# Performance work log

Measured on AMD Instinct MI355X. Metric: run time of the kernel, lower is better.

## Reference

```python
import jax, jax.numpy as jnp
import numpy as np

B, L, D = 1, 2048, 1024
H, E = 16, 64        # n_heads, d_head
ROT = E // 2         # rotary half-dim
FF = 4 * D
EPS = 1e-6
NEG = -1e30


def setup_inputs() -> dict:
    key = jax.random.key(0)
    ks = jax.random.split(key, 6)
    x = jax.random.normal(ks[0], (B, L, D), jnp.float32)
    theta = jax.random.uniform(ks[1], (B, H, L, ROT), jnp.float32) * (2.0 * np.pi)
    scale = jax.random.normal(ks[2], (B, D), jnp.float32) * 0.1
    w_in = jax.random.normal(ks[3], (7 * D, D), jnp.float32) * (D ** -0.5)
    w_out = jax.random.normal(ks[4], (D, 5 * D), jnp.float32) * ((5 * D) ** -0.5)
    attn_scale = jnp.full((2, H), 10.0, jnp.float32)
    return {"x": x, "theta": theta, "scale": scale,
            "w_in": w_in, "w_out": w_out, "attn_scale": attn_scale}


def _rope(t, cos, sin):
    # t: [b,h,l,E]; rotary applied to first 2*ROT dims (== E here, so no passthrough)
    t1, t2 = t[..., :ROT], t[..., ROT:2 * ROT]
    return jnp.concatenate([t1 * cos - t2 * sin, t2 * cos + t1 * sin], axis=-1)


def _forward(x, theta, scale, w_in, w_out, attn_scale):
    b, l, d = x.shape
    skip = x
    # AdaRMSNorm (no learned weight): rms-normalize then modulate by (1 + scale)
    xn = x * jax.lax.rsqrt(jnp.mean(x ** 2, axis=-1, keepdims=True) + EPS)
    xn = xn * (1.0 + scale[:, None, :])
    # fused QKV + MLP-up projection (torch Linear: y = x @ W.T)
    proj = jnp.einsum('bld,fd->blf', xn, w_in)       # [b,l,7d]
    qkv, up = proj[..., :3 * d], proj[..., 3 * d:]
    up = jax.nn.gelu(up, approximate=True)           # GELU(tanh)
    # 'b l (t nh e) -> t b nh l e'
    qkv = qkv.reshape(b, l, 3, H, E).transpose(2, 0, 3, 1, 4)
    q, k, v = qkv[0], qkv[1], qkv[2]
    # cosine-sim rescaling: q_h * sqrt(s_h)/||q||, k_h * sqrt(s_h)/||k||
    s = jnp.sqrt(attn_scale[0])[None, :, None, None]
    q = q * (s * jax.lax.rsqrt(jnp.sum(q ** 2, axis=-1, keepdims=True) + EPS))
    k = k * (s * jax.lax.rsqrt(jnp.sum(k ** 2, axis=-1, keepdims=True) + EPS))
    # rotary embedding
    cos, sin = jnp.cos(theta), jnp.sin(theta)
    q, k = _rope(q, cos, sin), _rope(k, cos, sin)
    # causal attention with scale = 1.0 (cosine-sim path)
    scores = jnp.einsum('bhqe,bhke->bhqk', q, k)
    causal = jnp.tril(jnp.ones((l, l), bool))
    scores = jnp.where(causal[None, None], scores, NEG)
    probs = jax.nn.softmax(scores, axis=-1)
    attn = jnp.einsum('bhqk,bhke->bhqe', probs, v)
    attn_out = attn.transpose(0, 2, 1, 3).reshape(b, l, d)  # 'b nh l e -> b l (nh e)'
    h = jnp.concatenate([attn_out, up], axis=-1)            # [b,l,5d]
    return jnp.einsum('blf,df->bld', h, w_out) + skip


def reference(x, theta, scale, w_in, w_out, attn_scale):
    return _forward(x, theta, scale, w_in, w_out, attn_scale)
```

## Files before the change

kernel.cpp:

```cpp
#include <hip/hip_runtime.h>

typedef unsigned short u16;
typedef unsigned int u32;
typedef __attribute__((ext_vector_type(8))) short bf16x8;
typedef __attribute__((ext_vector_type(8))) unsigned short u16x8;
typedef __attribute__((ext_vector_type(4))) float f32x4;
typedef __attribute__((ext_vector_type(16))) float f32x16;

#define L_SEQ 2048
#define DMODEL 1024
#define NHEAD 16
#define EHEAD 64
#define FPROJ 7168
#define FCAT 5120
#define NEGINF -1e30f
#define LOG2E 1.44269504088896f
#define EXP2F(x) __builtin_amdgcn_exp2f(x)

__device__ __forceinline__ u16 f2bf(float f) {
  union { float f; u32 u; } v; v.f = f;
  u32 r = v.u + 0x7FFFu + ((v.u >> 16) & 1u);
  return (u16)(r >> 16);
}
__device__ __forceinline__ float bf2f(u16 h) {
  union { u32 u; float f; } v; v.u = ((u32)h) << 16;
  return v.f;
}
__device__ __forceinline__ float gelu_f(float x) {
  float y = 0.7978845608028654f * (x + 0.044715f * x * x * x);
  float t = __expf(-2.0f * fabsf(y));
  float th = (1.0f - t) / (1.0f + t);
  th = (y < 0.0f) ? -th : th;
  return 0.5f * x * (1.0f + th);
}
__device__ __forceinline__ void gld16(void* lds, const void* g) {
  __builtin_amdgcn_global_load_lds((const __attribute__((address_space(1))) u32*)g,
                                   (__attribute__((address_space(3))) u32*)lds, 16, 0, 0);
}

__global__ __launch_bounds__(256) void cvt2_kernel(const float* __restrict__ a,
                                                   u16* __restrict__ oa, int na4,
                                                   const float* __restrict__ b,
                                                   u16* __restrict__ ob, int nb4) {
  int i = blockIdx.x * 256 + threadIdx.x;
  const float* src;
  u16* dst;
  int j;
  if (i < na4) {
    src = a; dst = oa; j = i;
  } else {
    j = i - na4;
    if (j >= nb4) return;
    src = b; dst = ob;
  }
  float4 v = ((const float4*)src)[j];
  ((u32*)dst)[2 * j] = (u32)f2bf(v.x) | ((u32)f2bf(v.y) << 16);
  ((u32*)dst)[2 * j + 1] = (u32)f2bf(v.z) | ((u32)f2bf(v.w) << 16);
}

__global__ __launch_bounds__(256) void rmsnorm_kernel(const float* __restrict__ x,
                                                      const float* __restrict__ scale,
                                                      u16* __restrict__ xn) {
  int row = blockIdx.x;
  const float4 v = ((const float4*)(x + (size_t)row * DMODEL))[threadIdx.x];
  float ss = v.x * v.x + v.y * v.y + v.z * v.z + v.w * v.w;
#pragma unroll
  for (int m = 1; m < 64; m <<= 1) ss += __shfl_xor(ss, m);
  __shared__ float ws[4];
  if ((threadIdx.x & 63) == 0) ws[threadIdx.x >> 6] = ss;
  __syncthreads();
  float tot = ws[0] + ws[1] + ws[2] + ws[3];
  float r = rsqrtf(tot * (1.0f / DMODEL) + 1e-6f);
  float4 sc = ((const float4*)scale)[threadIdx.x];
  u32 w0 = (u32)f2bf(v.x * r * (1.0f + sc.x)) | ((u32)f2bf(v.y * r * (1.0f + sc.y)) << 16);
  u32 w1 = (u32)f2bf(v.z * r * (1.0f + sc.z)) | ((u32)f2bf(v.w * r * (1.0f + sc.w)) << 16);
  u32* dst = (u32*)(xn + (size_t)row * DMODEL);
  dst[2 * threadIdx.x] = w0;
  dst[2 * threadIdx.x + 1] = w1;
}

__device__ __forceinline__ void stage_half(u16* lds, const u16* g, int K, int tid) {
#pragma unroll
  for (int i = 0; i < 2; ++i) {
    int idx = tid + i * 512;
    int r = idx >> 3;
    int gcb = ((idx & 7) << 4) ^ ((r & 7) << 4);
    gld16((char*)lds + idx * 16, (const char*)g + (size_t)r * K * 2 + gcb);
  }
}

#define GFENCE asm volatile("" ::: "memory")
#define VMW0 asm volatile("s_waitcnt vmcnt(0)" ::: "memory")
#define VMW2 asm volatile("s_waitcnt vmcnt(2)" ::: "memory")
#define ST_A(BUF, T, HALF) stage_half(sA + (BUF) * 16384 + (HALF) * 8192, \
    Ab + (size_t)((HALF) * 128) * K + (T) * 64, K, tid)
#define ST_B(BUF, T, HALF) stage_half(sB + (BUF) * 16384 + (HALF) * 8192, \
    Bb + (size_t)((HALF) * 128) * K + (T) * 64, K, tid)

#define PHASE(HM, KH, BUFB, DOVM, STCODE) do { \
    const char* ab_ = (const char*)sA + (BUFB) * 32768 + (HM) * 16384 + frow * 128 + ((KH) ? co1 : co0); \
    const char* bb_ = (const char*)sB + (BUFB) * 32768 + (wn * 32 + frow) * 128 + ((KH) ? co1 : co0); \
    bf16x8 af_[8], bv_[2]; \
    _Pragma("unroll") \
    for (int mr = 0; mr < 8; ++mr) af_[mr] = *(const bf16x8*)(ab_ + mr * 2048); \
    bv_[0] = *(const bf16x8*)(bb_); \
    bv_[1] = *(const bf16x8*)(bb_ + 2048); \
    GFENCE; \
    STCODE; \
    if (DOVM) VMW2; \
    __builtin_amdgcn_s_barrier(); \
    __builtin_amdgcn_s_setprio(1); \
    _Pragma("unroll") \
    for (int mr = 0; mr < 8; ++mr) { \
      acc[(HM) * 8 + mr][0] = __builtin_amdgcn_mfma_f32_16x16x32_bf16(af_[mr], bv_[0], acc[(HM) * 8 + mr][0], 0, 0, 0); \
      acc[(HM) * 8 + mr][1] = __builtin_amdgcn_mfma_f32_16x16x32_bf16(af_[mr], bv_[1], acc[(HM) * 8 + mr][1], 0, 0, 0); \
    } \
    __builtin_amdgcn_s_setprio(0); \
    __builtin_amdgcn_s_barrier(); \
  } while (0)

template <int OUTMODE>
__global__ __launch_bounds__(512, 2) void gemm256(const u16* __restrict__ A,
                                                  const u16* __restrict__ B,
                                                  u16* __restrict__ C0,
                                                  u16* __restrict__ C1,
                                                  int M, int N, int K) {
  __shared__ __align__(16) u16 smem[65536];
  u16* const sA = smem;
  u16* const sB = smem + 32768;
  const int tid = threadIdx.x;
  const int lane = tid & 63;
  const int wn = tid >> 6;
  const int frow = lane & 15;
  const int kbyte = ((lane >> 4) & 3) << 4;
  const int sw = (frow & 7) << 4;
  const int co0 = kbyte ^ sw;
  const int co1 = (64 | kbyte) ^ sw;

  const int nbx = N >> 8;
  const int nbm = (int)gridDim.x / nbx;
  const int v = (blockIdx.x & 7) * ((int)gridDim.x >> 3) + ((int)blockIdx.x >> 3);
  const int bm = v % nbm, bn = v / nbm;
  const int kper = K / (int)gridDim.y;
  const int kbeg = blockIdx.y * kper;
  const u16* Ab = A + (size_t)(bm * 256) * K + kbeg;
  const u16* Bb = B + (size_t)(bn * 256) * K + kbeg;

  f32x4 acc[16][2] = {};

  const int NT = kper >> 6;
  ST_A(0, 0, 0); ST_B(0, 0, 0); ST_B(0, 0, 1); ST_A(0, 0, 1); ST_A(1, 1, 0);
  VMW2;
  __builtin_amdgcn_s_barrier();

  for (int kt = 0; kt < NT; kt += 2) {
    const int t1 = kt + 1;
    const int t2 = (kt + 2 >= NT) ? kt + 2 - NT : kt + 2;
    const int t3 = (kt + 3 >= NT) ? kt + 3 - NT : kt + 3;
    PHASE(0, 0, 0, 0, ST_B(1, t1, 0));
    PHASE(0, 1, 0, 0, ST_B(1, t1, 1));
    PHASE(1, 0, 0, 0, ST_A(1, t1, 1));
    PHASE(1, 1, 0, 1, ST_A(0, t2, 0));
    PHASE(0, 0, 1, 0, ST_B(0, t2, 0));
    PHASE(0, 1, 1, 0, ST_B(0, t2, 1));
    PHASE(1, 0, 1, 0, ST_A(0, t2, 1));
    PHASE(1, 1, 1, 1, ST_A(1, t3, 0));
  }

  VMW0;
  __syncthreads();

  const int lr0 = (lane >> 4) * 4;
  const bool up = (OUTMODE == 1) && (bn >= 12);
  u16* const Cp2 = (OUTMODE == 2) ? C0 + (size_t)blockIdx.y * M * N : nullptr;

#pragma unroll
  for (int hm = 0; hm < 2; ++hm) {
#pragma unroll
    for (int m8 = 0; m8 < 8; ++m8) {
#pragma unroll
      for (int nr = 0; nr < 2; ++nr) {
        int col = wn * 32 + nr * 16 + frow;
#pragma unroll
        for (int r = 0; r < 4; ++r) {
          float vv = acc[hm * 8 + m8][nr][r];
          smem[(m8 * 16 + lr0 + r) * 272 + col] = f2bf(up ? gelu_f(vv) : vv);
        }
      }
    }
    __syncthreads();
#pragma unroll
    for (int j = 0; j < 8; ++j) {
      int row = j * 16 + (tid >> 5);
      int c16 = (tid & 31) * 8;
      u16x8 vv = *(const u16x8*)&smem[row * 272 + c16];
      int gr = bm * 256 + hm * 128 + row;
      int gc = bn * 256 + c16;
      if (OUTMODE == 1) {
        if (!up) *(u16x8*)(C0 + (size_t)gr * (3 * DMODEL) + gc) = vv;
        else     *(u16x8*)(C1 + (size_t)gr * FCAT + (gc - 2048)) = vv;
      } else {
        *(u16x8*)(Cp2 + (size_t)gr * N + gc) = vv;
      }
    }
    __syncthreads();
  }
}

__global__ __launch_bounds__(256) void combine8(const u16* __restrict__ part,
                                                const float* __restrict__ x,
                                                float* __restrict__ out) {
  size_t i = (size_t)(blockIdx.x * 256 + threadIdx.x) * 8;
  float4 x0 = *(const float4*)(x + i);
  float4 x1 = *(const float4*)(x + i + 4);
  float s[8] = {x0.x, x0.y, x0.z, x0.w, x1.x, x1.y, x1.z, x1.w};
#pragma unroll
  for (int p = 0; p < 8; ++p) {
    u16x8 v = *(const u16x8*)(part + (size_t)p * (L_SEQ * DMODEL) + i);
#pragma unroll
    for (int j = 0; j < 8; ++j) s[j] += bf2f(v[j]);
  }
  float4 o0 = {s[0], s[1], s[2], s[3]};
  float4 o1 = {s[4], s[5], s[6], s[7]};
  *(float4*)(out + i) = o0;
  *(float4*)(out + i + 4) = o1;
}

__global__ __launch_bounds__(256) void qkv_prep(const u16* __restrict__ proj,
                                                const float* __restrict__ theta,
                                                const float* __restrict__ attn_scale,
                                                u16* __restrict__ qb, u16* __restrict__ kb,
                                                u16* __restrict__ vb) {
  const int l = blockIdx.x * 4 + (threadIdx.x >> 6);
  const int hd = blockIdx.y;
  const int e = threadIdx.x & 63;
  const u16* pr = proj + (size_t)l * (3 * DMODEL) + hd * EHEAD + e;
  float q = bf2f(pr[0]);
  float k = bf2f(pr[DMODEL]);
  float v = bf2f(pr[2 * DMODEL]);
  float sq = q * q, sk = k * k;
#pragma unroll
  for (int m = 1; m < 64; m <<= 1) {
    sq += __shfl_xor(sq, m);
    sk += __shfl_xor(sk, m);
  }
  float s = sqrtf(attn_scale[hd]);
  q *= LOG2E * s * rsqrtf(sq + 1e-6f);
  k *= s * rsqrtf(sk + 1e-6f);
  float ang = theta[((size_t)hd * L_SEQ + l) * 32 + (e & 31)];
  float cs = __cosf(ang), sn = __sinf(ang);
  float qp = __shfl_xor(q, 32), kp = __shfl_xor(k, 32);
  float qr = (e < 32) ? (q * cs - qp * sn) : (q * cs + qp * sn);
  float kr = (e < 32) ? (k * cs - kp * sn) : (k * cs + kp * sn);
  size_t o = ((size_t)hd * L_SEQ + l) * EHEAD + e;
  qb[o] = f2bf(qr);
  kb[o] = f2bf(kr);
  vb[o] = f2bf(v);
}

__global__ __launch_bounds__(128, 4) void attn_kernel(const u16* __restrict__ qb,
                                                      const u16* __restrict__ kb,
                                                      const u16* __restrict__ vb,
                                                      u16* __restrict__ po,
                                                      float* __restrict__ pm,
                                                      float* __restrict__ pl) {
  const int bid = blockIdx.x;
  const int s = 31 - (bid >> 6);
  const int hd = (bid >> 2) & 15;
  const int c = bid & 3;
  const int tid = threadIdx.x;
  const int lane = tid & 63;
  const int w = tid >> 6;
  const int h = lane >> 5;
  const int ql = lane & 31;
  const int qg = s * 64 + w * 32 + ql;
  const int nt = s + 1;
  const int t0 = (c * nt) >> 2;
  const int t1 = ((c + 1) * nt) >> 2;

  __shared__ u16 sK[64 * 64];
  __shared__ u16 sVT[64 * 64];

  const u16* Kh = kb + (size_t)hd * L_SEQ * EHEAD;
  const u16* Vh = vb + (size_t)hd * L_SEQ * EHEAD;
  const u16* Qh = qb + (size_t)hd * L_SEQ * EHEAD;

  bf16x8 qf[4];
#pragma unroll
  for (int es = 0; es < 4; ++es)
    qf[es] = *(const bf16x8*)(Qh + (size_t)qg * EHEAD + es * 16 + h * 8);

  f32x16 oa[2] = {};
  float m = NEGINF, lsum = 0.0f;

  const int vk = (tid & 15) * 4;
  const int ve = (tid >> 4) * 8;

  for (int kt = t0; kt < t1; ++kt) {
    const int k0 = kt * 64;
    __syncthreads();
#pragma unroll
    for (int i = 0; i < 4; ++i) {
      int r = w * 32 + i * 8 + (lane >> 3);
      const u16* src = Kh + (size_t)(k0 + r) * EHEAD + (((lane & 7) ^ (r & 7)) << 3);
      gld16(sK + (w * 32 + i * 8) * 64 + lane * 8, src);
    }
    u16x8 vr[4];
#pragma unroll
    for (int j = 0; j < 4; ++j)
      vr[j] = *(const u16x8*)(Vh + (size_t)(k0 + vk + j) * EHEAD + ve);
#pragma unroll
    for (int e = 0; e < 8; ++e) {
      int row = ve + e;
      int boff = row * 128 + ((((vk >> 3) ^ (row & 7)) << 4) | ((vk & 4) << 1));
      ushort4 pv;
      pv.x = vr[0][e]; pv.y = vr[1][e]; pv.z = vr[2][e]; pv.w = vr[3][e];
      *(ushort4*)((char*)sVT + boff) = pv;
    }
    __syncthreads();

    f32x16 st[2];
#pragma unroll
    for (int t = 0; t < 2; ++t) {
      f32x16 a = {};
      __builtin_amdgcn_s_setprio(1);
#pragma unroll
      for (int es = 0; es < 4; ++es) {
        int row = t * 32 + ql;
        int boff = row * 128 + (((es * 2 + h) ^ (row & 7)) << 4);
        bf16x8 kf = *(const bf16x8*)((const char*)sK + boff);
        a = __builtin_amdgcn_mfma_f32_32x32x16_bf16(kf, qf[es], a, 0, 0, 0);
      }
      __builtin_amdgcn_s_setprio(0);
      st[t] = a;
    }

    float p[2][16];
    float mx = NEGINF;
    const bool edge = (kt == s);
#pragma unroll
    for (int t = 0; t < 2; ++t)
#pragma unroll
      for (int r = 0; r < 16; ++r) {
        float v = st[t][r];
        if (edge) {
          int kg = k0 + t * 32 + (r & 3) + ((r >> 2) << 3) + h * 4;
          v = (kg > qg) ? NEGINF : v;
        }
        p[t][r] = v;
        mx = fmaxf(mx, v);
      }
    mx = fmaxf(mx, __shfl_xor(mx, 32));
    if (!__all(mx - m <= 8.0f)) {
      float mnew = fmaxf(m, mx);
      float alpha = EXP2F(m - mnew);
      lsum *= alpha;
#pragma unroll
      for (int et = 0; et < 2; ++et)
#pragma unroll
        for (int r = 0; r < 16; ++r) oa[et][r] *= alpha;
      m = mnew;
    }
    float ps = 0.0f;
#pragma unroll
    for (int t = 0; t < 2; ++t)
#pragma unroll
      for (int r = 0; r < 16; ++r) {
        float e_ = EXP2F(p[t][r] - m);
        p[t][r] = e_;
        ps += e_;
      }
    ps += __shfl_xor(ps, 32);
    lsum += ps;

    u32 pk_[2][8];
#pragma unroll
    for (int t = 0; t < 2; ++t)
#pragma unroll
      for (int i = 0; i < 8; ++i)
        asm("v_cvt_pk_bf16_f32 %0, %1, %2" : "=v"(pk_[t][i]) : "v"(p[t][2 * i]), "v"(p[t][2 * i + 1]));

#pragma unroll
    for (int ks = 0; ks < 4; ++ks) {
      const int tp = ks >> 1, base = (ks & 1) * 4;
      u32 s0 = h ? pk_[tp][base + 0] : pk_[tp][base + 2];
      u32 s1 = h ? pk_[tp][base + 1] : pk_[tp][base + 3];
      u32 r0 = (u32)__shfl_xor((int)s0, 32);
      u32 r1 = (u32)__shfl_xor((int)s1, 32);
      union { u32 u[4]; bf16x8 v; } pf;
      pf.u[0] = h ? r0 : pk_[tp][base + 0];
      pf.u[1] = h ? r1 : pk_[tp][base + 1];
      pf.u[2] = h ? pk_[tp][base + 2] : r0;
      pf.u[3] = h ? pk_[tp][base + 3] : r1;
      __builtin_amdgcn_s_setprio(1);
#pragma unroll
      for (int et = 0; et < 2; ++et) {
        int row = et * 32 + ql;
        int boff = row * 128 + (((ks * 2 + h) ^ (row & 7)) << 4);
        bf16x8 vf = *(const bf16x8*)((const char*)sVT + boff);
        oa[et] = __builtin_amdgcn_mfma_f32_32x32x16_bf16(vf, pf.v, oa[et], 0, 0, 0);
      }
      __builtin_amdgcn_s_setprio(0);
    }
  }

  const size_t pidx = (size_t)(s * 16 + hd) * 4 + c;
  u16* orow = po + pidx * 4096 + (size_t)(w * 32 + ql) * 64;
#pragma unroll
  for (int et = 0; et < 2; ++et)
#pragma unroll
    for (int g = 0; g < 4; ++g) {
      ushort4 ov;
      ov.x = f2bf(oa[et][4 * g + 0]);
      ov.y = f2bf(oa[et][4 * g + 1]);
      ov.z = f2bf(oa[et][4 * g + 2]);
      ov.w = f2bf(oa[et][4 * g + 3]);
      *(ushort4*)(orow + et * 32 + g * 8 + h * 4) = ov;
    }
  if (h == 0) {
    pm[pidx * 64 + w * 32 + ql] = m;
    pl[pidx * 64 + w * 32 + ql] = lsum;
  }
}

__global__ __launch_bounds__(256) void attn_merge(const u16* __restrict__ po,
                                                  const float* __restrict__ pm,
                                                  const float* __restrict__ pl,
                                                  u16* __restrict__ hb) {
  const int sh = blockIdx.x;
  const int s = sh >> 4, hd = sh & 15;
  const int r = threadIdx.x >> 2;
  const int ec = (threadIdx.x & 3) << 4;
  float mc[4], wgt[4];
  float M = NEGINF;
#pragma unroll
  for (int c = 0; c < 4; ++c) {
    mc[c] = pm[(size_t)(sh * 4 + c) * 64 + r];
    M = fmaxf(M, mc[c]);
  }
  float L = 0.0f;
#pragma unroll
  for (int c = 0; c < 4; ++c) {
    wgt[c] = EXP2F(mc[c] - M);
    L += pl[(size_t)(sh * 4 + c) * 64 + r] * wgt[c];
  }
  float inv = 1.0f / L;
  float o[16] = {};
#pragma unroll
  for (int c = 0; c < 4; ++c) {
    const u16* pp = po + (size_t)(sh * 4 + c) * 4096 + r * 64 + ec;
    u16x8 v0 = *(const u16x8*)pp;
    u16x8 v1 = *(const u16x8*)(pp + 8);
#pragma unroll
    for (int j = 0; j < 8; ++j) {
      o[j] += wgt[c] * bf2f(v0[j]);
      o[8 + j] += wgt[c] * bf2f(v1[j]);
    }
  }
  u16* dst = hb + (size_t)(s * 64 + r) * FCAT + hd * EHEAD + ec;
  u16x8 out0, out1;
#pragma unroll
  for (int j = 0; j < 8; ++j) {
    out0[j] = f2bf(o[j] * inv);
    out1[j] = f2bf(o[8 + j] * inv);
  }
  *(u16x8*)dst = out0;
  *(u16x8*)(dst + 8) = out1;
}

extern "C" void kernel_launch(void* const* d_in, const int* in_sizes, int n_in,
                              void* d_out, int out_size, void* d_ws, size_t ws_size,
                              hipStream_t stream) {
  const float* x = (const float*)d_in[0];
  const float* theta = (const float*)d_in[1];
  const float* scale = (const float*)d_in[2];
  const float* w_in = (const float*)d_in[3];
  const float* w_out = (const float*)d_in[4];
  const float* attn_scale = (const float*)d_in[5];
  float* out = (float*)d_out;

  char* ws = (char*)d_ws;
  u16* w_out_b = (u16*)ws;   ws += (size_t)DMODEL * FCAT * 2;
  u16* hb = (u16*)ws;        ws += (size_t)L_SEQ * FCAT * 2;
  u16* xn = (u16*)ws;        ws += (size_t)L_SEQ * DMODEL * 2;
  u16* w_in_b = (u16*)ws;    ws += (size_t)FPROJ * DMODEL * 2;
  u16* proj = (u16*)ws;      ws += (size_t)L_SEQ * 3 * DMODEL * 2;
  u16* qb = (u16*)ws;        ws += (size_t)NHEAD * L_SEQ * EHEAD * 2;
  u16* kb = (u16*)ws;        ws += (size_t)NHEAD * L_SEQ * EHEAD * 2;
  u16* vb = (u16*)ws;        ws += (size_t)NHEAD * L_SEQ * EHEAD * 2;
  u16* po = xn;
  float* pm = (float*)(po + (size_t)512 * 4 * 4096);
  float* pl = pm + 512 * 4 * 64;
  u16* part = xn;

  const int na4 = FPROJ * DMODEL / 4, nb4 = DMODEL * FCAT / 4;
  cvt2_kernel<<<(na4 + nb4 + 255) / 256, 256, 0, stream>>>(w_in, w_in_b, na4,
                                                           w_out, w_out_b, nb4);
  rmsnorm_kernel<<<L_SEQ, 256, 0, stream>>>(x, scale, xn);
  gemm256<1><<<(L_SEQ / 256) * (FPROJ / 256), 512, 0, stream>>>(xn, w_in_b, proj, hb,
                                                                L_SEQ, FPROJ, DMODEL);
  qkv_prep<<<dim3(L_SEQ / 4, NHEAD), 256, 0, stream>>>(proj, theta, attn_scale, qb, kb, vb);
  attn_kernel<<<2048, 128, 0, stream>>>(qb, kb, vb, po, pm, pl);
  attn_merge<<<512, 256, 0, stream>>>(po, pm, pl, hb);
  gemm256<2><<<dim3((L_SEQ / 256) * (DMODEL / 256), 8), 512, 0, stream>>>(hb, w_out_b, part,
                                                                          nullptr, L_SEQ, DMODEL, FCAT);
  combine8<<<L_SEQ * DMODEL / 8 / 256, 256, 0, stream>>>(part, x, out);
}
```

Before: 138.9 us.

## Fuse QKV norm, RoPE and head split into projection GEMM epilogue

Removes the separate qkv_prep kernel and the intermediate proj buffer. The QKV GEMM epilogue now computes per-head L2 normalisation, scaling and rotary directly from the LDS-staged tile and writes q/k/v in head-major layout. A sin/cos table is built from theta inside the weight-conversion kernel, so the epilogue only reads precomputed pairs. This saves a launch and a round trip of the projection through global memory. In exchange the epilogue gets heavier, each thread processes a whole 64-wide row with a 64-element local array, which may raise register pressure, and the float2 table adds a 16 MB write and later read.

```diff
diff --git a/kernel.cpp b/kernel.cpp
--- a/kernel.cpp
+++ b/kernel.cpp
@@ -38,24 +38,36 @@
                                    (__attribute__((address_space(3))) u32*)lds, 16, 0, 0);
 }
 
-__global__ __launch_bounds__(256) void cvt2_kernel(const float* __restrict__ a,
+__global__ __launch_bounds__(256) void cvt3_kernel(const float* __restrict__ a,
                                                    u16* __restrict__ oa, int na4,
                                                    const float* __restrict__ b,
-                                                   u16* __restrict__ ob, int nb4) {
+                                                   u16* __restrict__ ob, int nb4,
+                                                   const float* __restrict__ theta,
+                                                   float2* __restrict__ tab, int nt4) {
   int i = blockIdx.x * 256 + threadIdx.x;
-  const float* src;
-  u16* dst;
-  int j;
-  if (i < na4) {
-    src = a; dst = oa; j = i;
-  } else {
-    j = i - na4;
-    if (j >= nb4) return;
-    src = b; dst = ob;
-  }
-  float4 v = ((const float4*)src)[j];
-  ((u32*)dst)[2 * j] = (u32)f2bf(v.x) | ((u32)f2bf(v.y) << 16);
-  ((u32*)dst)[2 * j + 1] = (u32)f2bf(v.z) | ((u32)f2bf(v.w) << 16);
+  if (i < na4 + nb4) {
+    const float* src;
+    u16* dst;
+    int j;
+    if (i < na4) { src = a; dst = oa; j = i; }
+    else         { src = b; dst = ob; j = i - na4; }
+    float4 v = ((const float4*)src)[j];
+    ((u32*)dst)[2 * j] = (u32)f2bf(v.x) | ((u32)f2bf(v.y) << 16);
+    ((u32*)dst)[2 * j + 1] = (u32)f2bf(v.z) | ((u32)f2bf(v.w) << 16);
+    return;
+  }
+  int j = i - na4 - nb4;
+  if (j >= nt4) return;
+  float4 t = ((const float4*)theta)[j];
+  float2 o0, o1, o2, o3;
+  __sincosf(t.x, &o0.y, &o0.x);
+  __sincosf(t.y, &o1.y, &o1.x);
+  __sincosf(t.z, &o2.y, &o2.x);
+  __sincosf(t.w, &o3.y, &o3.x);
+  tab[4 * j + 0] = o0;
+  tab[4 * j + 1] = o1;
+  tab[4 * j + 2] = o2;
+  tab[4 * j + 3] = o3;
 }
 
 __global__ __launch_bounds__(256) void rmsnorm_kernel(const float* __restrict__ x,
@@ -124,6 +136,11 @@
                                                   const u16* __restrict__ B,
                                                   u16* __restrict__ C0,
                                                   u16* __restrict__ C1,
+                                                  u16* __restrict__ qb,
+                                                  u16* __restrict__ kb,
+                                                  u16* __restrict__ vb,
+                                                  const float2* __restrict__ tab,
+                                                  const float* __restrict__ ascale,
                                                   int M, int N, int K) {
   __shared__ __align__(16) u16 smem[65536];
   u16* const sA = smem;
@@ -170,7 +187,6 @@
   VMW0;
   __syncthreads();
 
-  const int lr0 = (lane >> 4) * 4;
   const bool up = (OUTMODE == 1) && (bn >= 12);
   u16* const Cp2 = (OUTMODE == 2) ? C0 + (size_t)blockIdx.y * M * N : nullptr;
 
@@ -184,24 +200,68 @@
 #pragma unroll
         for (int r = 0; r < 4; ++r) {
           float vv = acc[hm * 8 + m8][nr][r];
-          smem[(m8 * 16 + lr0 + r) * 272 + col] = f2bf(up ? gelu_f(vv) : vv);
+          smem[(m8 * 16 + ((lane >> 4) * 4) + r) * 272 + col] = f2bf(up ? gelu_f(vv) : vv);
         }
       }
     }
     __syncthreads();
-#pragma unroll
-    for (int j = 0; j < 8; ++j) {
-      int row = j * 16 + (tid >> 5);
-      int c16 = (tid & 31) * 8;
-      u16x8 vv = *(const u16x8*)&smem[row * 272 + c16];
-      int gr = bm * 256 + hm * 128 + row;
-      int gc = bn * 256 + c16;
-      if (OUTMODE == 1) {
-        if (!up) *(u16x8*)(C0 + (size_t)gr * (3 * DMODEL) + gc) = vv;
-        else     *(u16x8*)(C1 + (size_t)gr * FCAT + (gc - 2048)) = vv;
-      } else {
-        *(u16x8*)(Cp2 + (size_t)gr * N + gc) = vv;
-      }
+
+    if (OUTMODE == 2) {
+#pragma unroll
+      for (int j = 0; j < 8; ++j) {
+        int row = j * 16 + (tid >> 5);
+        int c16 = (tid & 31) * 8;
+        u16x8 vv = *(const u16x8*)&smem[row * 272 + c16];
+        *(u16x8*)(Cp2 + (size_t)(bm * 256 + hm * 128 + row) * N + bn * 256 + c16) = vv;
+      }
+    } else if (up) {
+#pragma unroll
+      for (int j = 0; j < 8; ++j) {
+        int row = j * 16 + (tid >> 5);
+        int c16 = (tid & 31) * 8;
+        u16x8 vv = *(const u16x8*)&smem[row * 272 + c16];
+        *(u16x8*)(C1 + (size_t)(bm * 256 + hm * 128 + row) * FCAT + (bn * 256 + c16 - 2048)) = vv;
+      }
+    } else if (bn >= 8) {
+#pragma unroll
+      for (int j = 0; j < 8; ++j) {
+        int row = j * 16 + (tid >> 5);
+        int c16 = (tid & 31) * 8;
+        int gcv = bn * 256 + c16 - 2048;
+        int hd = gcv >> 6, e0 = gcv & 63;
+        int l = bm * 256 + hm * 128 + row;
+        u16x8 vv = *(const u16x8*)&smem[row * 272 + c16];
+        *(u16x8*)(vb + ((size_t)hd * L_SEQ + l) * 64 + e0) = vv;
+      }
+    } else {
+      int r = tid >> 2, ch = tid & 3;
+      int l = bm * 256 + hm * 128 + r;
+      int gc0 = bn * 256 + ch * 64;
+      int hd = (gc0 & 1023) >> 6;
+      const bool isq = (bn < 4);
+      const u16* lr = &smem[r * 272 + ch * 64];
+      float ss = 0.f;
+#pragma unroll
+      for (int j8 = 0; j8 < 8; ++j8) {
+        u16x8 vv = *(const u16x8*)(lr + j8 * 8);
+#pragma unroll
+        for (int e = 0; e < 8; ++e) { float f = bf2f(vv[e]); ss += f * f; }
+      }
+      float s = sqrtf(ascale[hd]) * rsqrtf(ss + 1e-6f);
+      if (isq) s *= LOG2E;
+      const float2* tp = tab + ((size_t)hd * L_SEQ + l) * 32;
+      u16 ob[64];
+#pragma unroll
+      for (int e = 0; e < 32; ++e) {
+        float2 cz = tp[e];
+        float x0 = bf2f(lr[e]) * s;
+        float x1 = bf2f(lr[e + 32]) * s;
+        ob[e] = f2bf(x0 * cz.x - x1 * cz.y);
+        ob[e + 32] = f2bf(x1 * cz.x + x0 * cz.y);
+      }
+      u16* dst = (isq ? qb : kb) + ((size_t)hd * L_SEQ + l) * 64;
+#pragma unroll
+      for (int j8 = 0; j8 < 8; ++j8) *(u16x8*)(dst + j8 * 8) = *(const u16x8*)(ob + j8 * 8);
     }
     __syncthreads();
   }
@@ -224,38 +284,6 @@
   float4 o1 = {s[4], s[5], s[6], s[7]};
   *(float4*)(out + i) = o0;
   *(float4*)(out + i + 4) = o1;
-}
-
-__global__ __launch_bounds__(256) void qkv_prep(const u16* __restrict__ proj,
-                                                const float* __restrict__ theta,
-                                                const float* __restrict__ attn_scale,
-                                                u16* __restrict__ qb, u16* __restrict__ kb,
-                                                u16* __restrict__ vb) {
-  const int l = blockIdx.x * 4 + (threadIdx.x >> 6);
-  const int hd = blockIdx.y;
-  const int e = threadIdx.x & 63;
-  const u16* pr = proj + (size_t)l * (3 * DMODEL) + hd * EHEAD + e;
-  float q = bf2f(pr[0]);
-  float k = bf2f(pr[DMODEL]);
-  float v = bf2f(pr[2 * DMODEL]);
-  float sq = q * q, sk = k * k;
-#pragma unroll
-  for (int m = 1; m < 64; m <<= 1) {
-    sq += __shfl_xor(sq, m);
-    sk += __shfl_xor(sk, m);
-  }
-  float s = sqrtf(attn_scale[hd]);
-  q *= LOG2E * s * rsqrtf(sq + 1e-6f);
-  k *= s * rsqrtf(sk + 1e-6f);
-  float ang = theta[((size_t)hd * L_SEQ + l) * 32 + (e & 31)];
-  float cs = __cosf(ang), sn = __sinf(ang);
-  float qp = __shfl_xor(q, 32), kp = __shfl_xor(k, 32);
-  float qr = (e < 32) ? (q * cs - qp * sn) : (q * cs + qp * sn);
-  float kr = (e < 32) ? (k * cs - kp * sn) : (k * cs + kp * sn);
-  size_t o = ((size_t)hd * L_SEQ + l) * EHEAD + e;
-  qb[o] = f2bf(qr);
-  kb[o] = f2bf(kr);
-  vb[o] = f2bf(v);
 }
 
 __global__ __launch_bounds__(128, 4) void attn_kernel(const u16* __restrict__ qb,
@@ -484,25 +512,26 @@
   u16* hb = (u16*)ws;        ws += (size_t)L_SEQ * FCAT * 2;
   u16* xn = (u16*)ws;        ws += (size_t)L_SEQ * DMODEL * 2;
   u16* w_in_b = (u16*)ws;    ws += (size_t)FPROJ * DMODEL * 2;
-  u16* proj = (u16*)ws;      ws += (size_t)L_SEQ * 3 * DMODEL * 2;
   u16* qb = (u16*)ws;        ws += (size_t)NHEAD * L_SEQ * EHEAD * 2;
   u16* kb = (u16*)ws;        ws += (size_t)NHEAD * L_SEQ * EHEAD * 2;
   u16* vb = (u16*)ws;        ws += (size_t)NHEAD * L_SEQ * EHEAD * 2;
+  float2* tab = (float2*)ws; ws += (size_t)NHEAD * L_SEQ * 32 * sizeof(float2);
   u16* po = xn;
   float* pm = (float*)(po + (size_t)512 * 4 * 4096);
   float* pl = pm + 512 * 4 * 64;
   u16* part = xn;
 
   const int na4 = FPROJ * DMODEL / 4, nb4 = DMODEL * FCAT / 4;
-  cvt2_kernel<<<(na4 + nb4 + 255) / 256, 256, 0, stream>>>(w_in, w_in_b, na4,
-                                                           w_out, w_out_b, nb4);
+  const int nt4 = NHEAD * L_SEQ * 32 / 4;
+  cvt3_kernel<<<(na4 + nb4 + nt4 + 255) / 256, 256, 0, stream>>>(
+      w_in, w_in_b, na4, w_out, w_out_b, nb4, theta, tab, nt4);
   rmsnorm_kernel<<<L_SEQ, 256, 0, stream>>>(x, scale, xn);
-  gemm256<1><<<(L_SEQ / 256) * (FPROJ / 256), 512, 0, stream>>>(xn, w_in_b, proj, hb,
-                                                                L_SEQ, FPROJ, DMODEL);
-  qkv_prep<<<dim3(L_SEQ / 4, NHEAD), 256, 0, stream>>>(proj, theta, attn_scale, qb, kb, vb);
+  gemm256<1><<<(L_SEQ / 256) * (FPROJ / 256), 512, 0, stream>>>(
+      xn, w_in_b, nullptr, hb, qb, kb, vb, tab, attn_scale, L_SEQ, FPROJ, DMODEL);
   attn_kernel<<<2048, 128, 0, stream>>>(qb, kb, vb, po, pm, pl);
   attn_merge<<<512, 256, 0, stream>>>(po, pm, pl, hb);
-  gemm256<2><<<dim3((L_SEQ / 256) * (DMODEL / 256), 8), 512, 0, stream>>>(hb, w_out_b, part,
-                                                                          nullptr, L_SEQ, DMODEL, FCAT);
+  gemm256<2><<<dim3((L_SEQ / 256) * (DMODEL / 256), 8), 512, 0, stream>>>(
+      hb, w_out_b, part, nullptr, nullptr, nullptr, nullptr, nullptr, nullptr,
+      L_SEQ, DMODEL, FCAT);
   combine8<<<L_SEQ * DMODEL / 8 / 256, 256, 0, stream>>>(part, x, out);
 }
```

New measurement: 139.6 us. About the same (+0.5%).

## Fuse weight conversion with rmsnorm and halve GEMM barriers per phase

Applied to the files above, without the earlier changes.

Merges the weight bf16 conversion and the RMSNorm into one launch, using block-index ranges to pick the role, which removes one kernel launch. In the GEMM main loop, each phase now issues a single barrier at its start instead of two. The vmcnt waits are redistributed to looser counts (6/4) on every other phase. This cuts barrier stalls, but the wait counts must still guarantee that LDS data has landed, so there is a risk of race conditions if the accounting is wrong.

```diff
diff --git a/kernel.cpp b/kernel.cpp
--- a/kernel.cpp
+++ b/kernel.cpp
@@ -38,30 +38,27 @@
                                    (__attribute__((address_space(3))) u32*)lds, 16, 0, 0);
 }
 
-__global__ __launch_bounds__(256) void cvt2_kernel(const float* __restrict__ a,
+__global__ __launch_bounds__(256) void prep_kernel(const float* __restrict__ a,
                                                    u16* __restrict__ oa, int na4,
                                                    const float* __restrict__ b,
-                                                   u16* __restrict__ ob, int nb4) {
-  int i = blockIdx.x * 256 + threadIdx.x;
-  const float* src;
-  u16* dst;
-  int j;
-  if (i < na4) {
-    src = a; dst = oa; j = i;
-  } else {
-    j = i - na4;
-    if (j >= nb4) return;
-    src = b; dst = ob;
-  }
-  float4 v = ((const float4*)src)[j];
-  ((u32*)dst)[2 * j] = (u32)f2bf(v.x) | ((u32)f2bf(v.y) << 16);
-  ((u32*)dst)[2 * j + 1] = (u32)f2bf(v.z) | ((u32)f2bf(v.w) << 16);
-}
-
-__global__ __launch_bounds__(256) void rmsnorm_kernel(const float* __restrict__ x,
-                                                      const float* __restrict__ scale,
-                                                      u16* __restrict__ xn) {
-  int row = blockIdx.x;
+                                                   u16* __restrict__ ob, int nb4,
+                                                   int ncvt,
+                                                   const float* __restrict__ x,
+                                                   const float* __restrict__ scale,
+                                                   u16* __restrict__ xn) {
+  if ((int)blockIdx.x < ncvt) {
+    int i = blockIdx.x * 256 + threadIdx.x;
+    const float* src;
+    u16* dst;
+    int j;
+    if (i < na4) { src = a; dst = oa; j = i; }
+    else { j = i - na4; if (j >= nb4) return; src = b; dst = ob; }
+    float4 v = ((const float4*)src)[j];
+    ((u32*)dst)[2 * j] = (u32)f2bf(v.x) | ((u32)f2bf(v.y) << 16);
+    ((u32*)dst)[2 * j + 1] = (u32)f2bf(v.z) | ((u32)f2bf(v.w) << 16);
+    return;
+  }
+  int row = blockIdx.x - ncvt;
   const float4 v = ((const float4*)(x + (size_t)row * DMODEL))[threadIdx.x];
   float ss = v.x * v.x + v.y * v.y + v.z * v.z + v.w * v.w;
 #pragma unroll
@@ -92,12 +89,15 @@
 #define GFENCE asm volatile("" ::: "memory")
 #define VMW0 asm volatile("s_waitcnt vmcnt(0)" ::: "memory")
 #define VMW2 asm volatile("s_waitcnt vmcnt(2)" ::: "memory")
+#define VMW4 asm volatile("s_waitcnt vmcnt(4)" ::: "memory")
+#define VMW6 asm volatile("s_waitcnt vmcnt(6)" ::: "memory")
 #define ST_A(BUF, T, HALF) stage_half(sA + (BUF) * 16384 + (HALF) * 8192, \
     Ab + (size_t)((HALF) * 128) * K + (T) * 64, K, tid)
 #define ST_B(BUF, T, HALF) stage_half(sB + (BUF) * 16384 + (HALF) * 8192, \
     Bb + (size_t)((HALF) * 128) * K + (T) * 64, K, tid)
 
-#define PHASE(HM, KH, BUFB, DOVM, STCODE) do { \
+#define PHASE(HM, KH, BUFB, WCODE, STCODE) do { \
+    __builtin_amdgcn_s_barrier(); \
     const char* ab_ = (const char*)sA + (BUFB) * 32768 + (HM) * 16384 + frow * 128 + ((KH) ? co1 : co0); \
     const char* bb_ = (const char*)sB + (BUFB) * 32768 + (wn * 32 + frow) * 128 + ((KH) ? co1 : co0); \
     bf16x8 af_[8], bv_[2]; \
@@ -107,8 +107,7 @@
     bv_[1] = *(const bf16x8*)(bb_ + 2048); \
     GFENCE; \
     STCODE; \
-    if (DOVM) VMW2; \
-    __builtin_amdgcn_s_barrier(); \
+    WCODE; \
     __builtin_amdgcn_s_setprio(1); \
     _Pragma("unroll") \
     for (int mr = 0; mr < 8; ++mr) { \
@@ -116,7 +115,6 @@
       acc[(HM) * 8 + mr][1] = __builtin_amdgcn_mfma_f32_16x16x32_bf16(af_[mr], bv_[1], acc[(HM) * 8 + mr][1], 0, 0, 0); \
     } \
     __builtin_amdgcn_s_setprio(0); \
-    __builtin_amdgcn_s_barrier(); \
   } while (0)
 
 template <int OUTMODE>
@@ -151,26 +149,24 @@
   const int NT = kper >> 6;
   ST_A(0, 0, 0); ST_B(0, 0, 0); ST_B(0, 0, 1); ST_A(0, 0, 1); ST_A(1, 1, 0);
   VMW2;
-  __builtin_amdgcn_s_barrier();
 
   for (int kt = 0; kt < NT; kt += 2) {
     const int t1 = kt + 1;
     const int t2 = (kt + 2 >= NT) ? kt + 2 - NT : kt + 2;
     const int t3 = (kt + 3 >= NT) ? kt + 3 - NT : kt + 3;
-    PHASE(0, 0, 0, 0, ST_B(1, t1, 0));
-    PHASE(0, 1, 0, 0, ST_B(1, t1, 1));
-    PHASE(1, 0, 0, 0, ST_A(1, t1, 1));
-    PHASE(1, 1, 0, 1, ST_A(0, t2, 0));
-    PHASE(0, 0, 1, 0, ST_B(0, t2, 0));
-    PHASE(0, 1, 1, 0, ST_B(0, t2, 1));
-    PHASE(1, 0, 1, 0, ST_A(0, t2, 1));
-    PHASE(1, 1, 1, 1, ST_A(1, t3, 0));
+    PHASE(0, 0, 0, , ST_B(1, t1, 0));
+    PHASE(0, 1, 0, VMW6, ST_B(1, t1, 1));
+    PHASE(1, 0, 0, , ST_A(1, t1, 1));
+    PHASE(1, 1, 0, VMW4, ST_A(0, t2, 0));
+    PHASE(0, 0, 1, , ST_B(0, t2, 0));
+    PHASE(0, 1, 1, VMW6, ST_B(0, t2, 1));
+    PHASE(1, 0, 1, , ST_A(0, t2, 1));
+    PHASE(1, 1, 1, VMW4, ST_A(1, t3, 0));
   }
 
   VMW0;
   __syncthreads();
 
-  const int lr0 = (lane >> 4) * 4;
   const bool up = (OUTMODE == 1) && (bn >= 12);
   u16* const Cp2 = (OUTMODE == 2) ? C0 + (size_t)blockIdx.y * M * N : nullptr;
 
@@ -184,7 +180,7 @@
 #pragma unroll
         for (int r = 0; r < 4; ++r) {
           float vv = acc[hm * 8 + m8][nr][r];
-          smem[(m8 * 16 + lr0 + r) * 272 + col] = f2bf(up ? gelu_f(vv) : vv);
+          smem[(m8 * 16 + ((lane >> 4) * 4) + r) * 272 + col] = f2bf(up ? gelu_f(vv) : vv);
         }
       }
     }
@@ -494,9 +490,9 @@
   u16* part = xn;
 
   const int na4 = FPROJ * DMODEL / 4, nb4 = DMODEL * FCAT / 4;
-  cvt2_kernel<<<(na4 + nb4 + 255) / 256, 256, 0, stream>>>(w_in, w_in_b, na4,
-                                                           w_out, w_out_b, nb4);
-  rmsnorm_kernel<<<L_SEQ, 256, 0, stream>>>(x, scale, xn);
+  const int ncvt = (na4 + nb4 + 255) / 256;
+  prep_kernel<<<ncvt + L_SEQ, 256, 0, stream>>>(w_in, w_in_b, na4, w_out, w_out_b, nb4,
+                                                ncvt, x, scale, xn);
   gemm256<1><<<(L_SEQ / 256) * (FPROJ / 256), 512, 0, stream>>>(xn, w_in_b, proj, hb,
                                                                 L_SEQ, FPROJ, DMODEL);
   qkv_prep<<<dim3(L_SEQ / 4, NHEAD), 256, 0, stream>>>(proj, theta, attn_scale, qb, kb, vb);
```

Measured after the change: 133.6 us. -3.8%, faster.
